# Performance work log

Measured on AMD Instinct MI355X. Metric: run time of the kernel, lower is better.

## Reference

```python
import jax, jax.numpy as jnp
import numpy as np

LN_EPS = 1e-5
N_NODES, N_EDGES, D_IN, D_HID, N_LAYERS = 50000, 800000, 512, 512, 3


def setup_inputs() -> dict:
    key = jax.random.key(0)
    k0, k1, k2 = jax.random.split(key, 3)
    x = jax.random.normal(k0, (N_NODES, D_IN), dtype=jnp.float32)
    edge_index = jax.random.randint(k1, (2, N_EDGES), 0, N_NODES, dtype=jnp.int32)
    # Glorot-ish scale so activations stay sane through the stack
    Ws = jax.random.normal(k2, (N_LAYERS, D_HID, D_HID), dtype=jnp.float32) / np.float32(np.sqrt(D_HID))
    bs = jnp.zeros((N_LAYERS, D_HID), dtype=jnp.float32)
    gammas = jnp.ones((N_LAYERS, D_HID), dtype=jnp.float32)
    betas = jnp.zeros((N_LAYERS, D_HID), dtype=jnp.float32)
    return {"x": x, "edge_index": edge_index, "Ws": Ws, "bs": bs, "gammas": gammas, "betas": betas}


def _layer_norm(v, gamma, beta):
    mu = jnp.mean(v, axis=-1, keepdims=True)
    vc = v - mu
    var = jnp.mean(vc * vc, axis=-1, keepdims=True)
    return gamma * vc * jax.lax.rsqrt(var + LN_EPS) + beta


def reference(x, edge_index, Ws, bs, gammas, betas):
    src, dst = edge_index[0], edge_index[1]
    n = x.shape[0]
    # GCN degrees with self-loops (graph is fixed across layers)
    deg = 1.0 + jax.ops.segment_sum(jnp.ones(src.shape[0], x.dtype), dst, num_segments=n)
    inv_sqrt = jax.lax.rsqrt(deg)
    enorm = (inv_sqrt[src] * inv_sqrt[dst])[:, None]  # [E,1] symmetric norm
    h = x
    for l in range(Ws.shape[0]):
        ht = h @ Ws[l] + bs[l]                               # [N, D] linear
        agg = jax.ops.segment_sum(ht[src] * enorm, dst, num_segments=n)
        agg = agg + ht / deg[:, None]                        # self-loop term
        # dropout is identity in eval mode; then LayerNorm -> ReLU
        h = jnp.maximum(_layer_norm(agg, gammas[l], betas[l]), 0.0)
    return h
```

## Files before the change

### kernel.cpp

```cpp
#include <hip/hip_runtime.h>

#define N_NODES 50000
#define N_EDGES 800000
#define D_FEAT 512
#define N_LAYERS 3
#define LN_EPS 1e-5f
#define M_PAD 50176
#define N_SBLK ((N_NODES + 255) / 256)
#define CSR_CAP (N_EDGES + 7 * N_NODES + 8)

typedef __attribute__((ext_vector_type(8))) _Float16 half8;
typedef __attribute__((ext_vector_type(4))) _Float16 half4;
typedef __attribute__((ext_vector_type(4))) float f32x4;

__device__ __forceinline__ void gl_lds16(const unsigned short* g, unsigned short* l) {
  __builtin_amdgcn_global_load_lds((const __attribute__((address_space(1))) unsigned int*)g,
                                   (__attribute__((address_space(3))) unsigned int*)l, 16, 0, 0);
}


__global__ __launch_bounds__(256) void count_deg_kernel(const int* __restrict__ ei,
                                                        int* __restrict__ cnt) {
  int e = blockIdx.x * 256 + threadIdx.x;
  if (e < N_EDGES) atomicAdd(&cnt[ei[N_EDGES + e]], 1);
}

__global__ __launch_bounds__(256) void block_sum_kernel(const int* __restrict__ cnt,
                                                        int* __restrict__ bsum) {
  int i = blockIdx.x * 256 + threadIdx.x;
  int v = (i < N_NODES) ? ((cnt[i] + 7) & ~7) : 0;
#pragma unroll
  for (int off = 32; off > 0; off >>= 1) v += __shfl_down(v, off);
  __shared__ int w[4];
  if ((threadIdx.x & 63) == 0) w[threadIdx.x >> 6] = v;
  __syncthreads();
  if (threadIdx.x == 0) bsum[blockIdx.x] = w[0] + w[1] + w[2] + w[3];
}

__global__ __launch_bounds__(256) void scan_bsum_kernel(const int* __restrict__ bsum,
                                                        int* __restrict__ boff,
                                                        int* __restrict__ rowoff) {
  __shared__ int sd[256];
  int t = threadIdx.x;
  int v = (t < N_SBLK) ? bsum[t] : 0;
  sd[t] = v;
  __syncthreads();
#pragma unroll
  for (int off = 1; off < 256; off <<= 1) {
    int x = (t >= off) ? sd[t - off] : 0;
    __syncthreads();
    sd[t] += x;
    __syncthreads();
  }
  if (t < N_SBLK) boff[t] = sd[t] - v;
  if (t == 255) rowoff[N_NODES] = sd[255];
}

__global__ __launch_bounds__(256) void scan_final_kernel(const int* __restrict__ cnt,
                                                         const int* __restrict__ boff,
                                                         int* __restrict__ rowoff,
                                                         float* __restrict__ inv_sqrt) {
  __shared__ int sd[256];
  int t = threadIdx.x;
  int i = blockIdx.x * 256 + t;
  int c = (i < N_NODES) ? cnt[i] : 0;
  int v = (c + 7) & ~7;
  sd[t] = v;
  __syncthreads();
#pragma unroll
  for (int off = 1; off < 256; off <<= 1) {
    int x = (t >= off) ? sd[t - off] : 0;
    __syncthreads();
    sd[t] += x;
    __syncthreads();
  }
  if (i < N_NODES) {
    rowoff[i] = boff[blockIdx.x] + sd[t] - v;
    inv_sqrt[i] = rsqrtf(1.0f + (float)c);
  }
}

__global__ __launch_bounds__(256) void fill_csr_kernel(const int* __restrict__ ei,
                                                       const int* __restrict__ rowoff,
                                                       int* __restrict__ cursor,
                                                       int2* __restrict__ csr_pk,
                                                       const float* __restrict__ inv_sqrt) {
  int e = blockIdx.x * 256 + threadIdx.x;
  if (e < N_EDGES) {
    int s = ei[e];
    int d = ei[N_EDGES + e];
    int p = atomicAdd(&cursor[d], 1);
    int2 pk;
    pk.x = s;
    pk.y = __float_as_int(inv_sqrt[s] * inv_sqrt[d]);
    csr_pk[rowoff[d] + p] = pk;
  }
}

__global__ __launch_bounds__(256) void pad_csr_kernel(const int* __restrict__ cnt,
                                                      const int* __restrict__ rowoff,
                                                      int2* __restrict__ csr_pk) {
  int n = blockIdx.x * 256 + threadIdx.x;
  if (n < N_NODES) {
    int deg = cnt[n];
    int b = rowoff[n] + deg;
    int e = rowoff[n + 1];
    int2 pk;
    pk.x = n;
    pk.y = 0;
    for (int i = b; i < e; ++i) csr_pk[i] = pk;
  }
}


__global__ __launch_bounds__(256) void convert_x_kernel(const float* __restrict__ x,
                                                        _Float16* __restrict__ Ah,
                                                        _Float16* __restrict__ Al) {
  size_t i4 = ((size_t)blockIdx.x * 256 + threadIdx.x) * 4;
  int row = (int)(i4 >> 9);
  half4 h, l;
  if (row < N_NODES) {
    float4 v = *(const float4*)(x + i4);
    h[0] = (_Float16)v.x; l[0] = (_Float16)(v.x - (float)h[0]);
    h[1] = (_Float16)v.y; l[1] = (_Float16)(v.y - (float)h[1]);
    h[2] = (_Float16)v.z; l[2] = (_Float16)(v.z - (float)h[2]);
    h[3] = (_Float16)v.w; l[3] = (_Float16)(v.w - (float)h[3]);
  } else {
    h[0] = h[1] = h[2] = h[3] = (_Float16)0.f;
    l[0] = l[1] = l[2] = l[3] = (_Float16)0.f;
  }
  *(half4*)(Ah + i4) = h;
  *(half4*)(Al + i4) = l;
}

__global__ __launch_bounds__(256) void wconv_kernel(const float* __restrict__ W,
                                                    _Float16* __restrict__ Bh) {
  __shared__ float t[64][65];
  int n0 = blockIdx.x * 64, k0 = blockIdx.y * 64;
  int tid = threadIdx.x;
  int c = tid & 63, r4 = tid >> 6;
#pragma unroll
  for (int r = 0; r < 64; r += 4)
    t[r4 + r][c] = W[(size_t)(k0 + r4 + r) * D_FEAT + n0 + c];
  __syncthreads();
#pragma unroll
  for (int r = 0; r < 64; r += 4) {
    float v = t[c][r4 + r];
    Bh[(size_t)(n0 + r4 + r) * D_FEAT + k0 + c] = (_Float16)v;
  }
}


__global__ __launch_bounds__(256, 3) void mfma_gemm_kernel(
    const _Float16* __restrict__ Ah, const _Float16* __restrict__ Al,
    const _Float16* __restrict__ Bh, const float* __restrict__ bias,
    _Float16* __restrict__ ht) {
  __shared__ unsigned short sAh[128 * 32], sAl[128 * 32], sBh[128 * 32];

  int tid = threadIdx.x;
  int wave = tid >> 6, lane = tid & 63;

  int id = blockIdx.y * 4 + blockIdx.x;
  int mrow = (id & 7) + 8 * (id >> 5);
  int ncol = (id >> 3) & 3;
  int n0 = ncol * 128, m0 = mrow * 128;

  int r0 = (wave * 2 + 0) * 16 + (lane >> 2);
  int r1 = (wave * 2 + 1) * 16 + (lane >> 2);
  int s0 = (lane & 3) ^ ((r0 >> 1) & 3);
  int s1 = (lane & 3) ^ ((r1 >> 1) & 3);
  size_t gA0 = (size_t)(m0 + r0) * D_FEAT + s0 * 8;
  size_t gA1 = (size_t)(m0 + r1) * D_FEAT + s1 * 8;
  size_t gB0 = (size_t)(n0 + r0) * D_FEAT + s0 * 8;
  size_t gB1 = (size_t)(n0 + r1) * D_FEAT + s1 * 8;
  int l0 = (wave * 2 + 0) * 512;
  int l1 = (wave * 2 + 1) * 512;

  int q = lane >> 4, fr = lane & 15;
  int wm = (wave >> 1) * 64, wn = (wave & 1) * 64;
  int aoff[4], boff[4];
#pragma unroll
  for (int i = 0; i < 4; ++i) {
    int row = wm + i * 16 + fr;
    aoff[i] = row * 32 + (q ^ ((row >> 1) & 3)) * 8;
  }
#pragma unroll
  for (int j = 0; j < 4; ++j) {
    int row = wn + j * 16 + fr;
    boff[j] = row * 32 + (q ^ ((row >> 1) & 3)) * 8;
  }

  f32x4 acc[4][4];
#pragma unroll
  for (int i = 0; i < 4; ++i)
#pragma unroll
    for (int j = 0; j < 4; ++j) acc[i][j] = (f32x4)0.0f;

  for (int k0 = 0; k0 < D_FEAT; k0 += 32) {
    gl_lds16((const unsigned short*)(Ah + gA0 + k0), sAh + l0);
    gl_lds16((const unsigned short*)(Ah + gA1 + k0), sAh + l1);
    gl_lds16((const unsigned short*)(Al + gA0 + k0), sAl + l0);
    gl_lds16((const unsigned short*)(Al + gA1 + k0), sAl + l1);
    gl_lds16((const unsigned short*)(Bh + gB0 + k0), sBh + l0);
    gl_lds16((const unsigned short*)(Bh + gB1 + k0), sBh + l1);
    __syncthreads();

    half8 ah[4], al[4], bh[4];
#pragma unroll
    for (int i = 0; i < 4; ++i) ah[i] = *(const half8*)(sAh + aoff[i]);
#pragma unroll
    for (int i = 0; i < 4; ++i) al[i] = *(const half8*)(sAl + aoff[i]);
#pragma unroll
    for (int j = 0; j < 4; ++j) bh[j] = *(const half8*)(sBh + boff[j]);
#pragma unroll
    for (int i = 0; i < 4; ++i)
#pragma unroll
      for (int j = 0; j < 4; ++j)
        acc[i][j] = __builtin_amdgcn_mfma_f32_16x16x32_f16(ah[i], bh[j], acc[i][j], 0, 0, 0);
#pragma unroll
    for (int i = 0; i < 4; ++i)
#pragma unroll
      for (int j = 0; j < 4; ++j)
        acc[i][j] = __builtin_amdgcn_mfma_f32_16x16x32_f16(al[i], bh[j], acc[i][j], 0, 0, 0);
    __syncthreads();
  }

  float bj[4];
#pragma unroll
  for (int j = 0; j < 4; ++j) bj[j] = bias[n0 + wn + j * 16 + fr];
#pragma unroll
  for (int i = 0; i < 4; ++i) {
    int gm0 = m0 + wm + i * 16 + q * 4;
#pragma unroll
    for (int j = 0; j < 4; ++j) {
      int gn = n0 + wn + j * 16 + fr;
#pragma unroll
      for (int r = 0; r < 4; ++r) {
        int gm = gm0 + r;
        if (gm < N_NODES)
          ht[(size_t)gm * D_FEAT + gn] = (_Float16)(acc[i][j][r] + bj[j]);
      }
    }
  }
}


template <bool LAST>
__global__ __launch_bounds__(256) void agg_ln_relu_kernel(
    const _Float16* __restrict__ ht, const int* __restrict__ rowoff,
    const int2* __restrict__ csr_pk, const float* __restrict__ inv_sqrt,
    const float* __restrict__ gamma, const float* __restrict__ beta,
    float* __restrict__ hout, _Float16* __restrict__ ph, _Float16* __restrict__ pl) {
  int n = blockIdx.x * 4 + (threadIdx.x >> 6);
  int lane = threadIdx.x & 63;
  int c8 = lane * 8;

  half8 vself = *(const half8*)(ht + (size_t)n * D_FEAT + c8);
  float isn = inv_sqrt[n];

  int beg = rowoff[n];
  int end = rowoff[n + 1];
  int ng = (end - beg) >> 3;
  const int2* cp = csr_pk + beg;

  float acc[8];
#pragma unroll
  for (int k = 0; k < 8; ++k) acc[k] = 0.f;

  if (ng > 0) {
    int2 p[8];
#pragma unroll
    for (int k = 0; k < 8; ++k) p[k] = cp[k];
    for (int g = 0; g < ng; ++g) {
      half8 v[8];
      float w[8];
#pragma unroll
      for (int k = 0; k < 8; ++k) {
        v[k] = *(const half8*)(ht + (size_t)p[k].x * D_FEAT + c8);
        w[k] = __int_as_float(p[k].y);
      }
#pragma unroll
      for (int k = 0; k < 8; ++k) p[k] = cp[(size_t)(g + 1) * 8 + k];
#pragma unroll
      for (int k = 0; k < 8; ++k)
#pragma unroll
        for (int j = 0; j < 8; ++j) acc[j] = fmaf(w[k], (float)v[k][j], acc[j]);
    }
  }
  {
    float w = isn * isn;
#pragma unroll
    for (int k = 0; k < 8; ++k) acc[k] = fmaf(w, (float)vself[k], acc[k]);
  }

  float s = 0.f, s2 = 0.f;
#pragma unroll
  for (int k = 0; k < 8; ++k) { s += acc[k]; s2 += acc[k] * acc[k]; }
#pragma unroll
  for (int off = 32; off > 0; off >>= 1) {
    s += __shfl_xor(s, off);
    s2 += __shfl_xor(s2, off);
  }

  const float inv_d = 1.0f / (float)D_FEAT;
  float mu = s * inv_d;
  float var = s2 * inv_d - mu * mu;
  float rstd = rsqrtf(var + LN_EPS);

  float4 g0 = *(const float4*)(gamma + c8);
  float4 g1 = *(const float4*)(gamma + c8 + 4);
  float4 b0 = *(const float4*)(beta + c8);
  float4 b1 = *(const float4*)(beta + c8 + 4);
  float gg[8] = {g0.x, g0.y, g0.z, g0.w, g1.x, g1.y, g1.z, g1.w};
  float bb[8] = {b0.x, b0.y, b0.z, b0.w, b1.x, b1.y, b1.z, b1.w};

  float o[8];
#pragma unroll
  for (int k = 0; k < 8; ++k)
    o[k] = fmaxf(gg[k] * (acc[k] - mu) * rstd + bb[k], 0.f);

  if (LAST) {
    *(float4*)(hout + (size_t)n * D_FEAT + c8) = make_float4(o[0], o[1], o[2], o[3]);
    *(float4*)(hout + (size_t)n * D_FEAT + c8 + 4) = make_float4(o[4], o[5], o[6], o[7]);
  } else {
    half8 h, l;
#pragma unroll
    for (int k = 0; k < 8; ++k) {
      _Float16 hh = (_Float16)o[k];
      h[k] = hh;
      l[k] = (_Float16)(o[k] - (float)hh);
    }
    size_t off = (size_t)n * D_FEAT + c8;
    *(half8*)(ph + off) = h;
    *(half8*)(pl + off) = l;
  }
}


extern "C" void kernel_launch(void* const* d_in, const int* in_sizes, int n_in,
                              void* d_out, int out_size, void* d_ws, size_t ws_size,
                              hipStream_t stream) {
  const float* x      = (const float*)d_in[0];
  const int*   ei     = (const int*)d_in[1];
  const float* Ws     = (const float*)d_in[2];
  const float* bs     = (const float*)d_in[3];
  const float* gammas = (const float*)d_in[4];
  const float* betas  = (const float*)d_in[5];
  float* out = (float*)d_out;

  _Float16* Ah  = (_Float16*)d_ws;
  _Float16* Al  = Ah + (size_t)M_PAD * D_FEAT;
  _Float16* Bth = Al + (size_t)M_PAD * D_FEAT;
  _Float16* htb = Bth + (size_t)D_FEAT * D_FEAT;
  int2* csr_pk  = (int2*)(htb + (size_t)N_NODES * D_FEAT);
  float* inv_sqrt = (float*)(csr_pk + CSR_CAP);
  int* deg_cnt = (int*)(inv_sqrt + N_NODES);
  int* rowoff  = deg_cnt + N_NODES;
  int* cursor  = rowoff + (N_NODES + 1);
  int* bsum    = cursor + N_NODES;
  int* boff    = bsum + N_SBLK;

  hipMemsetAsync(deg_cnt, 0, N_NODES * sizeof(int), stream);
  hipMemsetAsync(cursor, 0, N_NODES * sizeof(int), stream);

  count_deg_kernel<<<(N_EDGES + 255) / 256, 256, 0, stream>>>(ei, deg_cnt);
  block_sum_kernel<<<N_SBLK, 256, 0, stream>>>(deg_cnt, bsum);
  scan_bsum_kernel<<<1, 256, 0, stream>>>(bsum, boff, rowoff);
  scan_final_kernel<<<N_SBLK, 256, 0, stream>>>(deg_cnt, boff, rowoff, inv_sqrt);
  fill_csr_kernel<<<(N_EDGES + 255) / 256, 256, 0, stream>>>(ei, rowoff, cursor,
                                                             csr_pk, inv_sqrt);
  pad_csr_kernel<<<N_SBLK, 256, 0, stream>>>(deg_cnt, rowoff, csr_pk);

  convert_x_kernel<<<(M_PAD * D_FEAT / 4) / 256, 256, 0, stream>>>(x, Ah, Al);

  dim3 ggrid(D_FEAT / 128, M_PAD / 128);
  for (int l = 0; l < N_LAYERS; ++l) {
    wconv_kernel<<<dim3(8, 8), 256, 0, stream>>>(Ws + (size_t)l * D_FEAT * D_FEAT, Bth);
    mfma_gemm_kernel<<<ggrid, 256, 0, stream>>>(Ah, Al, Bth, bs + (size_t)l * D_FEAT, htb);
    if (l < N_LAYERS - 1) {
      agg_ln_relu_kernel<false><<<N_NODES / 4, 256, 0, stream>>>(
          htb, rowoff, csr_pk, inv_sqrt, gammas + (size_t)l * D_FEAT,
          betas + (size_t)l * D_FEAT, nullptr, Ah, Al);
    } else {
      agg_ln_relu_kernel<true><<<N_NODES / 4, 256, 0, stream>>>(
          htb, rowoff, csr_pk, inv_sqrt, gammas + (size_t)l * D_FEAT,
          betas + (size_t)l * D_FEAT, out, nullptr, nullptr);
    }
  }
}
```

Baseline: 847.7 us.

## Double-buffer GEMM LDS tiles and use nontemporal loads/stores in aggregation

Splits the MFMA GEMM's shared-memory tiles into two stages, so the next K-slice's global-to-LDS copies overlap with the current slice's MFMAs. The single-buffered loop exposed load latency every iteration. It also switches the output and CSR streams to nontemporal stores and loads, and restructures the edge loop to load neighbor features before prefetching the next edge group. The cost is doubled LDS use per block, and nontemporal stores of ht may reduce its cache residency before the gather kernel reads it.

```diff
diff --git a/kernel.cpp b/kernel.cpp
--- a/kernel.cpp
+++ b/kernel.cpp
@@ -155,7 +155,8 @@
     const _Float16* __restrict__ Ah, const _Float16* __restrict__ Al,
     const _Float16* __restrict__ Bh, const float* __restrict__ bias,
     _Float16* __restrict__ ht) {
-  __shared__ unsigned short sAh[128 * 32], sAl[128 * 32], sBh[128 * 32];
+  __shared__ unsigned short sAh0[128 * 32], sAl0[128 * 32], sBh0[128 * 32];
+  __shared__ unsigned short sAh1[128 * 32], sAl1[128 * 32], sBh1[128 * 32];
 
   int tid = threadIdx.x;
   int wave = tid >> 6, lane = tid & 63;
@@ -196,34 +197,47 @@
 #pragma unroll
     for (int j = 0; j < 4; ++j) acc[i][j] = (f32x4)0.0f;
 
-  for (int k0 = 0; k0 < D_FEAT; k0 += 32) {
-    gl_lds16((const unsigned short*)(Ah + gA0 + k0), sAh + l0);
-    gl_lds16((const unsigned short*)(Ah + gA1 + k0), sAh + l1);
-    gl_lds16((const unsigned short*)(Al + gA0 + k0), sAl + l0);
-    gl_lds16((const unsigned short*)(Al + gA1 + k0), sAl + l1);
-    gl_lds16((const unsigned short*)(Bh + gB0 + k0), sBh + l0);
-    gl_lds16((const unsigned short*)(Bh + gB1 + k0), sBh + l1);
-    __syncthreads();
-
-    half8 ah[4], al[4], bh[4];
-#pragma unroll
-    for (int i = 0; i < 4; ++i) ah[i] = *(const half8*)(sAh + aoff[i]);
-#pragma unroll
-    for (int i = 0; i < 4; ++i) al[i] = *(const half8*)(sAl + aoff[i]);
-#pragma unroll
-    for (int j = 0; j < 4; ++j) bh[j] = *(const half8*)(sBh + boff[j]);
-#pragma unroll
-    for (int i = 0; i < 4; ++i)
-#pragma unroll
-      for (int j = 0; j < 4; ++j)
-        acc[i][j] = __builtin_amdgcn_mfma_f32_16x16x32_f16(ah[i], bh[j], acc[i][j], 0, 0, 0);
-#pragma unroll
-    for (int i = 0; i < 4; ++i)
-#pragma unroll
-      for (int j = 0; j < 4; ++j)
-        acc[i][j] = __builtin_amdgcn_mfma_f32_16x16x32_f16(al[i], bh[j], acc[i][j], 0, 0, 0);
-    __syncthreads();
-  }
+#define STAGE(S, K)                                                      \
+  do {                                                                   \
+    gl_lds16((const unsigned short*)(Ah + gA0 + (K)), sAh##S + l0);      \
+    gl_lds16((const unsigned short*)(Ah + gA1 + (K)), sAh##S + l1);      \
+    gl_lds16((const unsigned short*)(Al + gA0 + (K)), sAl##S + l0);      \
+    gl_lds16((const unsigned short*)(Al + gA1 + (K)), sAl##S + l1);      \
+    gl_lds16((const unsigned short*)(Bh + gB0 + (K)), sBh##S + l0);      \
+    gl_lds16((const unsigned short*)(Bh + gB1 + (K)), sBh##S + l1);      \
+  } while (0)
+
+#define COMPUTE(S)                                                                        \
+  do {                                                                                    \
+    half8 ah[4], al[4], bh[4];                                                            \
+    _Pragma("unroll") for (int i = 0; i < 4; ++i) ah[i] =                                 \
+        *(const half8*)(sAh##S + aoff[i]);                                                \
+    _Pragma("unroll") for (int i = 0; i < 4; ++i) al[i] =                                 \
+        *(const half8*)(sAl##S + aoff[i]);                                                \
+    _Pragma("unroll") for (int j = 0; j < 4; ++j) bh[j] =                                 \
+        *(const half8*)(sBh##S + boff[j]);                                                \
+    _Pragma("unroll") for (int i = 0; i < 4; ++i)                                         \
+        _Pragma("unroll") for (int j = 0; j < 4; ++j) acc[i][j] =                         \
+            __builtin_amdgcn_mfma_f32_16x16x32_f16(ah[i], bh[j], acc[i][j], 0, 0, 0);     \
+    _Pragma("unroll") for (int i = 0; i < 4; ++i)                                         \
+        _Pragma("unroll") for (int j = 0; j < 4; ++j) acc[i][j] =                         \
+            __builtin_amdgcn_mfma_f32_16x16x32_f16(al[i], bh[j], acc[i][j], 0, 0, 0);     \
+  } while (0)
+
+  STAGE(0, 0);
+  __syncthreads();
+#pragma unroll
+  for (int kk = 0; kk < 8; ++kk) {
+    int k0 = kk * 64;
+    STAGE(1, k0 + 32);
+    COMPUTE(0);
+    __syncthreads();
+    if (kk < 7) STAGE(0, k0 + 64);
+    COMPUTE(1);
+    __syncthreads();
+  }
+#undef STAGE
+#undef COMPUTE
 
   float bj[4];
 #pragma unroll
@@ -238,7 +252,8 @@
       for (int r = 0; r < 4; ++r) {
         int gm = gm0 + r;
         if (gm < N_NODES)
-          ht[(size_t)gm * D_FEAT + gn] = (_Float16)(acc[i][j][r] + bj[j]);
+          __builtin_nontemporal_store((_Float16)(acc[i][j][r] + bj[j]),
+                                      ht + (size_t)gm * D_FEAT + gn);
       }
     }
   }
@@ -261,30 +276,43 @@
   int beg = rowoff[n];
   int end = rowoff[n + 1];
   int ng = (end - beg) >> 3;
-  const int2* cp = csr_pk + beg;
+  const long long* cpq = (const long long*)(csr_pk + beg);
 
   float acc[8];
 #pragma unroll
   for (int k = 0; k < 8; ++k) acc[k] = 0.f;
 
   if (ng > 0) {
-    int2 p[8];
-#pragma unroll
-    for (int k = 0; k < 8; ++k) p[k] = cp[k];
+    int px[8];
+    float pw[8];
+#pragma unroll
+    for (int k = 0; k < 8; ++k) {
+      long long raw = __builtin_nontemporal_load(cpq + k);
+      px[k] = (int)raw;
+      pw[k] = __int_as_float((int)(raw >> 32));
+    }
     for (int g = 0; g < ng; ++g) {
       half8 v[8];
-      float w[8];
+#pragma unroll
+      for (int k = 0; k < 8; ++k)
+        v[k] = *(const half8*)(ht + (size_t)px[k] * D_FEAT + c8);
+      int nx[8];
+      float nw[8];
 #pragma unroll
       for (int k = 0; k < 8; ++k) {
-        v[k] = *(const half8*)(ht + (size_t)p[k].x * D_FEAT + c8);
-        w[k] = __int_as_float(p[k].y);
+        long long raw = __builtin_nontemporal_load(cpq + (size_t)(g + 1) * 8 + k);
+        nx[k] = (int)raw;
+        nw[k] = __int_as_float((int)(raw >> 32));
       }
 #pragma unroll
-      for (int k = 0; k < 8; ++k) p[k] = cp[(size_t)(g + 1) * 8 + k];
-#pragma unroll
       for (int k = 0; k < 8; ++k)
 #pragma unroll
-        for (int j = 0; j < 8; ++j) acc[j] = fmaf(w[k], (float)v[k][j], acc[j]);
+        for (int j = 0; j < 8; ++j) acc[j] = fmaf(pw[k], (float)v[k][j], acc[j]);
+#pragma unroll
+      for (int k = 0; k < 8; ++k) {
+        px[k] = nx[k];
+        pw[k] = nw[k];
+      }
     }
   }
   {
@@ -320,8 +348,10 @@
     o[k] = fmaxf(gg[k] * (acc[k] - mu) * rstd + bb[k], 0.f);
 
   if (LAST) {
-    *(float4*)(hout + (size_t)n * D_FEAT + c8) = make_float4(o[0], o[1], o[2], o[3]);
-    *(float4*)(hout + (size_t)n * D_FEAT + c8 + 4) = make_float4(o[4], o[5], o[6], o[7]);
+    f32x4 o0 = {o[0], o[1], o[2], o[3]};
+    f32x4 o1 = {o[4], o[5], o[6], o[7]};
+    __builtin_nontemporal_store(o0, (f32x4*)(hout + (size_t)n * D_FEAT + c8));
+    __builtin_nontemporal_store(o1, (f32x4*)(hout + (size_t)n * D_FEAT + c8 + 4));
   } else {
     half8 h, l;
 #pragma unroll
@@ -331,8 +361,8 @@
       l[k] = (_Float16)(o[k] - (float)hh);
     }
     size_t off = (size_t)n * D_FEAT + c8;
-    *(half8*)(ph + off) = h;
-    *(half8*)(pl + off) = l;
+    __builtin_nontemporal_store(h, (half8*)(ph + off));
+    __builtin_nontemporal_store(l, (half8*)(pl + off));
   }
 }
 
```

Result: slower. 934.2 us (+10.2%).
